# Kernel optimization log

Measured on AMD Instinct MI355X. Metric: run time of the kernel, lower is better.

Reference implementation:

```python
import jax, jax.numpy as jnp
import numpy as np

DECAY = 0.99
EPS = 1e-05
NUM_EMBEDDINGS = 2048
EMBEDDING_DIM = 512


def setup_inputs() -> dict:
    key = jax.random.key(0)
    k1, k2 = jax.random.split(key)
    z_e = jax.random.normal(k1, (16, 4096, EMBEDDING_DIM), dtype=jnp.float32)
    embedding = jax.random.normal(k2, (NUM_EMBEDDINGS, EMBEDDING_DIM), dtype=jnp.float32)
    cluster_size = jnp.zeros((NUM_EMBEDDINGS,), dtype=jnp.float32)
    embed_avg = embedding  # buffer initialized as a clone of embedding
    return {"z_e": z_e, "embedding": embedding, "cluster_size": cluster_size, "embed_avg": embed_avg}


def reference(z_e, embedding, cluster_size, embed_avg):
    K, D = embedding.shape
    flat = z_e.reshape(-1, D)  # [N, D]
    dist = (jnp.sum(flat * flat, axis=1, keepdims=True)
            - 2.0 * flat @ embedding.T
            + jnp.sum(embedding * embedding, axis=1))
    idx = jnp.argmin(dist, axis=1)  # [N] int
    z_q_raw = embedding[idx].reshape(z_e.shape)

    # EMA cluster statistics (training path). one_hot.T @ flat == segment_sum
    counts = jax.ops.segment_sum(jnp.ones_like(idx, dtype=flat.dtype), idx, num_segments=K)
    embed_sum = jax.ops.segment_sum(flat, idx, num_segments=K)  # [K, D]
    new_cluster_size = DECAY * cluster_size + (1.0 - DECAY) * counts
    new_embed_avg = DECAY * embed_avg + (1.0 - DECAY) * embed_sum
    n = jnp.sum(new_cluster_size)
    cs_smoothed = (new_cluster_size + EPS) / (n + K * EPS) * n
    new_embedding = new_embed_avg / cs_smoothed[:, None]

    # straight-through estimator
    z_q = z_e + jax.lax.stop_gradient(z_q_raw - z_e)
    commit_loss = jnp.mean((jax.lax.stop_gradient(z_e) - z_q) ** 2)
    codebook_loss = jnp.mean((z_e - jax.lax.stop_gradient(z_q)) ** 2)
    vq_loss = codebook_loss + 0.25 * commit_loss
    return (z_q, idx, vq_loss, new_embedding, new_cluster_size, new_embed_avg)
```

## Files before the change

kernel.cpp:

```cpp
#include <hip/hip_runtime.h>

typedef unsigned short ushort_t;
typedef unsigned int u32;
typedef unsigned long long u64;
typedef __attribute__((ext_vector_type(8))) short bf16x8;
typedef __attribute__((ext_vector_type(4))) float f32x4;

#define N_ROWS 65536
#define K_EMB  2048
#define D_DIM  512
#define OFF_ZQ   0
#define OFF_IDX  33554432
#define OFF_LOSS 33619968
#define OFF_EMB  33619969
#define OFF_NCS  34668545
#define OFF_NEA  34670593
#define TAU 1.5f
#define CHUNK 128
#define MAXCHUNK 2560

__device__ __forceinline__ ushort_t f2bf(float f) {
  u32 u = __float_as_uint(f);
  u32 r = (u + 0x7fffu + ((u >> 16) & 1u)) >> 16;
  return (ushort_t)r;
}
__device__ __forceinline__ float bf2f(ushort_t h) { return __uint_as_float(((u32)h) << 16); }
__device__ __forceinline__ u32 f2mono(float f) {
  u32 u = __float_as_uint(f);
  return (u & 0x80000000u) ? ~u : (u | 0x80000000u);
}
__device__ __forceinline__ float unmono(u32 m) {
  u32 u = (m & 0x80000000u) ? (m & 0x7fffffffu) : ~m;
  return __uint_as_float(u);
}
__device__ __forceinline__ void glds16(const void* g, void* l) {
  __builtin_amdgcn_global_load_lds((const __attribute__((address_space(1))) u32*)g,
                                   (__attribute__((address_space(3))) u32*)l, 16, 0, 0);
}

__global__ void prep_z_kernel(const float* __restrict__ ze, ushort_t* __restrict__ xh,
                              float* __restrict__ counts, float* __restrict__ lossws)
{
  int gid = blockIdx.x * 256 + threadIdx.x;
  const float4* zin = (const float4*)ze;
  ushort4* xh4 = (ushort4*)xh;
  for (int g = gid; g < (N_ROWS * D_DIM / 4); g += 8192 * 256) {
    float4 v = zin[g];
    ushort4 h;
    h.x = f2bf(v.x); h.y = f2bf(v.y); h.z = f2bf(v.z); h.w = f2bf(v.w);
    xh4[g] = h;
  }
  if (gid < K_EMB) counts[gid] = 0.0f;
  if (gid == 0) lossws[0] = 0.0f;
}

__global__ void prep_e_kernel(const float* __restrict__ emb, ushort_t* __restrict__ eh,
                              float* __restrict__ enorm)
{
  int w = threadIdx.x >> 6, l = threadIdx.x & 63;
  int k = blockIdx.x * 4 + w;
  const float4* row = (const float4*)(emb + (size_t)k * D_DIM);
  float4 a = row[l * 2], b = row[l * 2 + 1];
  ushort4 h0, h1;
  h0.x = f2bf(a.x); h0.y = f2bf(a.y); h0.z = f2bf(a.z); h0.w = f2bf(a.w);
  h1.x = f2bf(b.x); h1.y = f2bf(b.y); h1.z = f2bf(b.z); h1.w = f2bf(b.w);
  ((ushort4*)(eh + (size_t)k * D_DIM))[l * 2] = h0;
  ((ushort4*)(eh + (size_t)k * D_DIM))[l * 2 + 1] = h1;
  float s = a.x*a.x + a.y*a.y + a.z*a.z + a.w*a.w + b.x*b.x + b.y*b.y + b.z*b.z + b.w*b.w;
  #pragma unroll
  for (int off = 32; off >= 1; off >>= 1) s += __shfl_xor(s, off);
  if (l == 0) enorm[k] = s;
}

#define MERGE4(s1,s2,s3,s4,o1,o2,o3,o4) do {                        \
    u32 x1 = min(s1,o4), x2 = min(s2,o3), x3 = min(s3,o2), x4 = min(s4,o1); \
    u32 t1 = min(x1,x3), t3 = max(x1,x3), t2 = min(x2,x4), t4 = max(x2,x4); \
    s1 = min(t1,t2); s2 = max(t1,t2); s3 = min(t3,t4); s4 = max(t3,t4);     \
  } while (0)

__global__ __launch_bounds__(256, 4)
void dist_gemm(const ushort_t* __restrict__ xh, const ushort_t* __restrict__ eh,
               const float* __restrict__ enorm, u32* __restrict__ list)
{
  __shared__ ushort_t Ah[128 * 64];
  __shared__ ushort_t Bh[128 * 64];
  const int t = threadIdx.x;
  const int w = t >> 6, l = t & 63;
  const int li = l & 15, lg = l >> 4;
  const int bx = blockIdx.x;
  const int rt = bx >> 4, ct = bx & 15;
  const int row0 = rt << 7, col0 = ct << 7;
  const int wr = (w >> 1) << 6, wc = (w & 1) << 6;

  f32x4 zero4 = {0.f, 0.f, 0.f, 0.f};
  f32x4 acc[4][4];
  #pragma unroll
  for (int m = 0; m < 4; ++m)
    #pragma unroll
    for (int n = 0; n < 4; ++n) acc[m][n] = zero4;

  const int Gbase = (w << 6) + l;
  for (int kit = 0; kit < 8; ++kit) {
    const int kb = kit << 7;
    #pragma unroll
    for (int i = 0; i < 4; ++i) {
      int G = (i << 8) + Gbase;
      int r = G >> 3, gp = G & 7;
      int cb = gp ^ (r & 7);
      size_t gA = ((size_t)(row0 + r) << 10) + kb + (cb << 4);
      size_t gB = ((size_t)(col0 + r) << 10) + kb + (cb << 4);
      int ld = ((i << 8) + (w << 6)) << 4;
      glds16((const char*)xh + gA, (char*)Ah + ld);
      glds16((const char*)eh + gB, (char*)Bh + ld);
    }
    __syncthreads();
    #pragma unroll
    for (int kblk = 0; kblk < 2; ++kblk) {
      bf16x8 fah[4], fbh[4];
      #pragma unroll
      for (int m = 0; m < 4; ++m) {
        int r = wr + (m << 4) + li;
        int c = (kblk << 2) + lg;
        int off = (r << 7) + ((c ^ (r & 7)) << 4);
        fah[m] = *(const bf16x8*)((const char*)Ah + off);
      }
      #pragma unroll
      for (int n = 0; n < 4; ++n) {
        int r = wc + (n << 4) + li;
        int c = (kblk << 2) + lg;
        int off = (r << 7) + ((c ^ (r & 7)) << 4);
        fbh[n] = *(const bf16x8*)((const char*)Bh + off);
      }
      #pragma unroll
      for (int m = 0; m < 4; ++m)
        #pragma unroll
        for (int n = 0; n < 4; ++n)
          acc[m][n] = __builtin_amdgcn_mfma_f32_16x16x32_bf16(fah[m], fbh[n], acc[m][n], 0, 0, 0);
    }
    __syncthreads();
  }

  float en[4];
  #pragma unroll
  for (int n = 0; n < 4; ++n) en[n] = enorm[col0 + wc + (n << 4) + li];

  u32* epi = (u32*)Ah;
  #pragma unroll
  for (int m = 0; m < 4; ++m) {
    #pragma unroll
    for (int i = 0; i < 4; ++i) {
      int lrow = wr + (m << 4) + (lg << 2) + i;
      u32 s1 = 0xFFFFFFFFu, s2 = 0xFFFFFFFFu, s3 = 0xFFFFFFFFu, s4 = 0xFFFFFFFFu;
      #pragma unroll
      for (int n = 0; n < 4; ++n) {
        float dist = en[n] - 2.0f * acc[m][n][i];
        u32 ent = ((f2mono(dist) >> 11) << 11) | (u32)(col0 + wc + (n << 4) + li);
        if (ent < s1)      { s4 = s3; s3 = s2; s2 = s1; s1 = ent; }
        else if (ent < s2) { s4 = s3; s3 = s2; s2 = ent; }
        else if (ent < s3) { s4 = s3; s3 = ent; }
        else if (ent < s4) { s4 = ent; }
      }
      #pragma unroll
      for (int off = 8; off >= 1; off >>= 1) {
        u32 o1 = __shfl_xor(s1, off);
        u32 o2 = __shfl_xor(s2, off);
        u32 o3 = __shfl_xor(s3, off);
        u32 o4 = __shfl_xor(s4, off);
        MERGE4(s1, s2, s3, s4, o1, o2, o3, o4);
      }
      if (li == 0) {
        u32* p = epi + (lrow << 3) + ((w & 1) << 2);
        p[0] = s1; p[1] = s2; p[2] = s3; p[3] = s4;
      }
    }
  }
  __syncthreads();
  if (t < 128) {
    u32* pa = epi + (t << 3);
    u32 s1 = pa[0], s2 = pa[1], s3 = pa[2], s4 = pa[3];
    u32 o1 = pa[4], o2 = pa[5], o3 = pa[6], o4 = pa[7];
    MERGE4(s1, s2, s3, s4, o1, o2, o3, o4);
    uint4 v; v.x = s1; v.y = s2; v.z = s3; v.w = s4;
    *(uint4*)(list + (((size_t)(row0 + t)) << 6) + (ct << 2)) = v;
  }
}

__global__ void finalize_kernel(const u32* __restrict__ list, const float* __restrict__ ze,
                                const float* __restrict__ emb, int* __restrict__ wsidx,
                                float* __restrict__ counts)
{
  int w = threadIdx.x >> 6, l = threadIdx.x & 63;
  int row = blockIdx.x * 4 + w;
  u32 ent = list[(((size_t)row) << 6) + l];
  u32 e1 = ent;
  #pragma unroll
  for (int off = 32; off >= 1; off >>= 1) e1 = min(e1, __shfl_xor(e1, off));
  float d1 = unmono(e1 & ~2047u);
  float dl = unmono(ent & ~2047u);
  u64 mask = __ballot(dl < d1 + TAU);
  int idx;
  if (__popcll(mask) <= 1) {
    idx = (int)(e1 & 2047u);
  } else {
    double bd = 1e300; int bc = 0x7fffffff;
    const float* xr = ze + (((size_t)row) << 9);
    u64 mm = mask;
    while (mm) {
      int j = (int)(__ffsll((long long)mm) - 1);
      mm &= mm - 1;
      u32 cj = __shfl(ent, j);
      int col = (int)(cj & 2047u);
      const float* er = emb + (((size_t)col) << 9);
      double s = 0.0;
      #pragma unroll
      for (int q = 0; q < 8; ++q) {
        double df = (double)xr[(l << 3) + q] - (double)er[(l << 3) + q];
        s += df * df;
      }
      #pragma unroll
      for (int off = 32; off >= 1; off >>= 1) s += __shfl_xor(s, off);
      if (s < bd || (s == bd && col < bc)) { bd = s; bc = col; }
    }
    idx = bc;
  }
  if (l == 0) {
    wsidx[row] = idx;
    atomicAdd(&counts[idx], 1.0f);
  }
}

__global__ void scan_kernel(const float* __restrict__ counts, u32* __restrict__ offsets,
                            u32* __restrict__ cursor, u32* __restrict__ chunkinfo,
                            u32* __restrict__ ntotal)
{
  int t = threadIdx.x;
  int c[8]; int s = 0;
  #pragma unroll
  for (int i = 0; i < 8; ++i) { c[i] = (int)counts[t * 8 + i]; s += c[i]; }
  __shared__ int ts[256];
  ts[t] = s; __syncthreads();
  for (int off = 1; off < 256; off <<= 1) {
    int v = (t >= off) ? ts[t - off] : 0;
    __syncthreads();
    ts[t] += v;
    __syncthreads();
  }
  int run = ts[t] - s;
  int nch[8]; int ns = 0;
  #pragma unroll
  for (int i = 0; i < 8; ++i) {
    offsets[t * 8 + i] = (u32)run;
    cursor[t * 8 + i] = 0;
    run += c[i];
    nch[i] = (c[i] + CHUNK - 1) / CHUNK;
    ns += nch[i];
  }
  __shared__ int ts2[256];
  ts2[t] = ns; __syncthreads();
  for (int off = 1; off < 256; off <<= 1) {
    int v = (t >= off) ? ts2[t - off] : 0;
    __syncthreads();
    ts2[t] += v;
    __syncthreads();
  }
  int cb = ts2[t] - ns;
  #pragma unroll
  for (int i = 0; i < 8; ++i)
    for (int cc = 0; cc < nch[i]; ++cc)
      chunkinfo[cb++] = (u32)(t * 8 + i) | ((u32)cc << 11);
  if (t == 255) *ntotal = (u32)ts2[255];
}

__global__ void scatter_kernel(const int* __restrict__ wsidx, const u32* __restrict__ offsets,
                               u32* __restrict__ cursor, u32* __restrict__ sorted)
{
  int row = blockIdx.x * 256 + threadIdx.x;
  int idx = wsidx[row];
  u32 pos = atomicAdd(&cursor[idx], 1u);
  sorted[offsets[idx] + pos] = (u32)row;
}

__global__ void zesum_kernel(float* __restrict__ esum)
{
  int gid = blockIdx.x * 256 + threadIdx.x;
  for (int i = gid; i < K_EMB * D_DIM; i += 1024 * 256) esum[i] = 0.0f;
}

__global__ __launch_bounds__(256)
void zq_seg_kernel(const float* __restrict__ ze, const float* __restrict__ emb,
                   const u32* __restrict__ offsets, const float* __restrict__ counts,
                   const u32* __restrict__ sorted, const u32* __restrict__ chunkinfo,
                   const u32* __restrict__ ntotal, float* __restrict__ o_zq,
                   float* __restrict__ o_idx, float* __restrict__ esum,
                   float* __restrict__ lossws)
{
  int cid = blockIdx.x;
  if (cid >= (int)*ntotal) return;
  u32 rec = chunkinfo[cid];
  int k = rec & 2047, c = (int)(rec >> 11);
  int ctotal = (int)counts[k];
  int base = (int)offsets[k] + c * CHUNK;
  int cnt = min(ctotal - c * CHUNK, CHUNK);
  bool multi = ctotal > CHUNK;
  int t = threadIdx.x, w = t >> 6, l = t & 63;
  __shared__ u32 srow[CHUNK];
  __shared__ float sacc[4 * 512];
  __shared__ float sloss[4];
  if (t < cnt) srow[t] = sorted[base + t];
  __syncthreads();
  const float4* e4 = (const float4*)(emb + ((size_t)k << 9));
  float4 ev0 = e4[l * 2], ev1 = e4[l * 2 + 1];
  float a0x=0,a0y=0,a0z=0,a0w=0,a1x=0,a1y=0,a1z=0,a1w=0;
  float lacc = 0.f;
  for (int r = w; r < cnt; r += 4) {
    int row = (int)srow[r];
    const float4* z4 = (const float4*)(ze + ((size_t)row << 9));
    float4 zv0 = z4[l * 2], zv1 = z4[l * 2 + 1];
    float4 q0, q1;
    q0.x = zv0.x + (ev0.x - zv0.x);
    q0.y = zv0.y + (ev0.y - zv0.y);
    q0.z = zv0.z + (ev0.z - zv0.z);
    q0.w = zv0.w + (ev0.w - zv0.w);
    q1.x = zv1.x + (ev1.x - zv1.x);
    q1.y = zv1.y + (ev1.y - zv1.y);
    q1.z = zv1.z + (ev1.z - zv1.z);
    q1.w = zv1.w + (ev1.w - zv1.w);
    float4* zq4 = (float4*)(o_zq + ((size_t)row << 9));
    zq4[l * 2] = q0; zq4[l * 2 + 1] = q1;
    float dx = zv0.x - q0.x, dy = zv0.y - q0.y, dz = zv0.z - q0.z, dw = zv0.w - q0.w;
    lacc += dx*dx + dy*dy + dz*dz + dw*dw;
    dx = zv1.x - q1.x; dy = zv1.y - q1.y; dz = zv1.z - q1.z; dw = zv1.w - q1.w;
    lacc += dx*dx + dy*dy + dz*dz + dw*dw;
    a0x += zv0.x; a0y += zv0.y; a0z += zv0.z; a0w += zv0.w;
    a1x += zv1.x; a1y += zv1.y; a1z += zv1.z; a1w += zv1.w;
    if (l == 0) o_idx[row] = (float)k;
  }
  #pragma unroll
  for (int off = 32; off >= 1; off >>= 1) lacc += __shfl_xor(lacc, off);
  if (l == 0) sloss[w] = lacc;
  float* sa = sacc + w * 512 + l * 8;
  sa[0]=a0x; sa[1]=a0y; sa[2]=a0z; sa[3]=a0w; sa[4]=a1x; sa[5]=a1y; sa[6]=a1z; sa[7]=a1w;
  __syncthreads();
  #pragma unroll
  for (int j = 0; j < 2; ++j) {
    int col = t * 2 + j;
    float v = sacc[col] + sacc[512 + col] + sacc[1024 + col] + sacc[1536 + col];
    if (multi) atomicAdd(&esum[((size_t)k << 9) + col], v);
    else       esum[((size_t)k << 9) + col] = v;
  }
  if (t == 0) atomicAdd(lossws, sloss[0] + sloss[1] + sloss[2] + sloss[3]);
}

__global__ void d1_kernel(const float* __restrict__ cs, const float* __restrict__ counts,
                          float* __restrict__ o_ncs, float* __restrict__ inv,
                          const float* __restrict__ lossws, float* __restrict__ o_loss)
{
  int t = threadIdx.x;
  float ncs[8]; float s = 0.0f;
  #pragma unroll
  for (int i = 0; i < 8; ++i) {
    int k = t + (i << 8);
    float v = 0.99f * cs[k] + 0.01f * counts[k];
    ncs[i] = v; o_ncs[k] = v; s += v;
  }
  __shared__ float red[256];
  red[t] = s; __syncthreads();
  for (int h = 128; h >= 1; h >>= 1) { if (t < h) red[t] += red[t + h]; __syncthreads(); }
  float n = red[0];
  float denom = n + 2048.0f * 1e-5f;
  #pragma unroll
  for (int i = 0; i < 8; ++i) {
    int k = t + (i << 8);
    float sm = (ncs[i] + 1e-5f) / denom * n;
    inv[k] = 1.0f / sm;
  }
  if (t == 0) o_loss[0] = lossws[0] * 1.25f / 33554432.0f;
}

__global__ void d2_kernel(const float* __restrict__ ea, const float* __restrict__ inv,
                          float* __restrict__ o_emb, float* __restrict__ o_nea)
{
  int gid = blockIdx.x * 256 + threadIdx.x;
  for (int i = gid; i < K_EMB * D_DIM; i += 1024 * 256) {
    float es = o_emb[i];
    float nea = 0.99f * ea[i] + 0.01f * es;
    o_nea[i] = nea;
    o_emb[i] = nea * inv[i >> 9];
  }
}

extern "C" void kernel_launch(void* const* d_in, const int* in_sizes, int n_in,
                              void* d_out, int out_size, void* d_ws, size_t ws_size,
                              hipStream_t stream)
{
  const float* ze  = (const float*)d_in[0];
  const float* emb = (const float*)d_in[1];
  const float* cs  = (const float*)d_in[2];
  const float* ea  = (const float*)d_in[3];
  float* out = (float*)d_out;
  float* o_zq   = out + OFF_ZQ;
  float* o_idx  = out + OFF_IDX;
  float* o_loss = out + OFF_LOSS;
  float* o_emb  = out + OFF_EMB;
  float* o_ncs  = out + OFF_NCS;
  float* o_nea  = out + OFF_NEA;
  ushort_t* xh = (ushort_t*)d_out;
  u32* list = (u32*)(out + 16777216);
  char* ws = (char*)d_ws;
  ushort_t* ehp = (ushort_t*)ws;
  int* wsidx    = (int*)(ws + 2097152);
  float* counts = (float*)(ws + 2097152 + 262144);
  float* enorm  = counts + 2048;
  float* inv    = enorm + 2048;
  float* lossws = inv + 2048;
  u32* offsets  = (u32*)(lossws + 64);
  u32* cursor   = offsets + 2048;
  u32* sorted   = cursor + 2048;
  u32* chunkinfo= sorted + 65536;
  u32* ntotal   = chunkinfo + MAXCHUNK;

  prep_z_kernel<<<8192, 256, 0, stream>>>(ze, xh, counts, lossws);
  prep_e_kernel<<<512, 256, 0, stream>>>(emb, ehp, enorm);
  dist_gemm<<<8192, 256, 0, stream>>>(xh, ehp, enorm, list);
  finalize_kernel<<<16384, 256, 0, stream>>>(list, ze, emb, wsidx, counts);
  scan_kernel<<<1, 256, 0, stream>>>(counts, offsets, cursor, chunkinfo, ntotal);
  scatter_kernel<<<256, 256, 0, stream>>>(wsidx, offsets, cursor, sorted);
  zesum_kernel<<<1024, 256, 0, stream>>>(o_emb);
  zq_seg_kernel<<<MAXCHUNK, 256, 0, stream>>>(ze, emb, offsets, counts, sorted,
                                              chunkinfo, ntotal, o_zq, o_idx, o_emb, lossws);
  d1_kernel<<<1, 256, 0, stream>>>(cs, counts, o_ncs, inv, lossws, o_loss);
  d2_kernel<<<1024, 256, 0, stream>>>(ea, inv, o_emb, o_nea);
}
```

Before: 415.4 us.

## Fuse top-4 candidate selection across all codebook tiles inside distance GEMM

Each GEMM block now covers 128 rows against every 128-column codebook tile and keeps a running top-4 of packed distance|index keys in registers. It writes one uint4 per row instead of 64 candidate entries per row, which removes the large candidate-list write and reread and simplifies finalize to checking 4 candidates. The zeroing of the embedding sum is also restricted to clusters that are empty or larger than one chunk. Risks: the grid shrinks to 512 blocks with a two-per-CU launch bound, so the GPU may be less full. The monotone float-to-uint mapping is dropped, so ordering is only correct when distances are non-negative, which holds for these inputs but not in general.

```diff
diff --git a/kernel.cpp b/kernel.cpp
--- a/kernel.cpp
+++ b/kernel.cpp
@@ -24,19 +24,16 @@
   u32 r = (u + 0x7fffu + ((u >> 16) & 1u)) >> 16;
   return (ushort_t)r;
 }
-__device__ __forceinline__ float bf2f(ushort_t h) { return __uint_as_float(((u32)h) << 16); }
-__device__ __forceinline__ u32 f2mono(float f) {
-  u32 u = __float_as_uint(f);
-  return (u & 0x80000000u) ? ~u : (u | 0x80000000u);
-}
-__device__ __forceinline__ float unmono(u32 m) {
-  u32 u = (m & 0x80000000u) ? (m & 0x7fffffffu) : ~m;
-  return __uint_as_float(u);
-}
 __device__ __forceinline__ void glds16(const void* g, void* l) {
   __builtin_amdgcn_global_load_lds((const __attribute__((address_space(1))) u32*)g,
                                    (__attribute__((address_space(3))) u32*)l, 16, 0, 0);
 }
+
+#define MERGE4(s1,s2,s3,s4,o1,o2,o3,o4) do {                        \
+    u32 x1 = min(s1,o4), x2 = min(s2,o3), x3 = min(s3,o2), x4 = min(s4,o1); \
+    u32 t1 = min(x1,x3), t3 = max(x1,x3), t2 = min(x2,x4), t4 = max(x2,x4); \
+    s1 = min(t1,t2); s2 = max(t1,t2); s3 = min(t3,t4); s4 = max(t3,t4);     \
+  } while (0)
 
 __global__ void prep_z_kernel(const float* __restrict__ ze, ushort_t* __restrict__ xh,
                               float* __restrict__ counts, float* __restrict__ lossws)
@@ -72,149 +69,175 @@
   if (l == 0) enorm[k] = s;
 }
 
-#define MERGE4(s1,s2,s3,s4,o1,o2,o3,o4) do {                        \
-    u32 x1 = min(s1,o4), x2 = min(s2,o3), x3 = min(s3,o2), x4 = min(s4,o1); \
-    u32 t1 = min(x1,x3), t3 = max(x1,x3), t2 = min(x2,x4), t4 = max(x2,x4); \
-    s1 = min(t1,t2); s2 = max(t1,t2); s3 = min(t3,t4); s4 = max(t3,t4);     \
-  } while (0)
-
-__global__ __launch_bounds__(256, 4)
+__global__ __launch_bounds__(256, 2)
 void dist_gemm(const ushort_t* __restrict__ xh, const ushort_t* __restrict__ eh,
-               const float* __restrict__ enorm, u32* __restrict__ list)
+               const float* __restrict__ enorm, uint4* __restrict__ list)
 {
   __shared__ ushort_t Ah[128 * 64];
   __shared__ ushort_t Bh[128 * 64];
   const int t = threadIdx.x;
   const int w = t >> 6, l = t & 63;
   const int li = l & 15, lg = l >> 4;
-  const int bx = blockIdx.x;
-  const int rt = bx >> 4, ct = bx & 15;
-  const int row0 = rt << 7, col0 = ct << 7;
+  const int row0 = blockIdx.x << 7;
   const int wr = (w >> 1) << 6, wc = (w & 1) << 6;
 
-  f32x4 zero4 = {0.f, 0.f, 0.f, 0.f};
-  f32x4 acc[4][4];
-  #pragma unroll
-  for (int m = 0; m < 4; ++m)
-    #pragma unroll
-    for (int n = 0; n < 4; ++n) acc[m][n] = zero4;
+  u32 cand[16][4];
+  #pragma unroll
+  for (int mi = 0; mi < 16; ++mi) {
+    cand[mi][0] = 0xFFFFFFFFu; cand[mi][1] = 0xFFFFFFFFu;
+    cand[mi][2] = 0xFFFFFFFFu; cand[mi][3] = 0xFFFFFFFFu;
+  }
 
   const int Gbase = (w << 6) + l;
-  for (int kit = 0; kit < 8; ++kit) {
-    const int kb = kit << 7;
-    #pragma unroll
-    for (int i = 0; i < 4; ++i) {
-      int G = (i << 8) + Gbase;
-      int r = G >> 3, gp = G & 7;
-      int cb = gp ^ (r & 7);
-      size_t gA = ((size_t)(row0 + r) << 10) + kb + (cb << 4);
-      size_t gB = ((size_t)(col0 + r) << 10) + kb + (cb << 4);
-      int ld = ((i << 8) + (w << 6)) << 4;
-      glds16((const char*)xh + gA, (char*)Ah + ld);
-      glds16((const char*)eh + gB, (char*)Bh + ld);
+
+  for (int ct = 0; ct < 16; ++ct) {
+    const int col0 = ct << 7;
+    float en0 = enorm[col0 + wc + 0  + li];
+    float en1 = enorm[col0 + wc + 16 + li];
+    float en2 = enorm[col0 + wc + 32 + li];
+    float en3 = enorm[col0 + wc + 48 + li];
+
+    f32x4 acc[4][4];
+    #pragma unroll
+    for (int m = 0; m < 4; ++m)
+      #pragma unroll
+      for (int n = 0; n < 4; ++n) acc[m][n] = (f32x4){0.f, 0.f, 0.f, 0.f};
+
+    for (int kit = 0; kit < 8; ++kit) {
+      const int kb = kit << 7;
+      #pragma unroll
+      for (int i = 0; i < 4; ++i) {
+        int G = (i << 8) + Gbase;
+        int r = G >> 3, gp = G & 7;
+        int cb = gp ^ (r & 7);
+        size_t gA = ((size_t)(row0 + r) << 10) + kb + (cb << 4);
+        size_t gB = ((size_t)(col0 + r) << 10) + kb + (cb << 4);
+        int ld = ((i << 8) + (w << 6)) << 4;
+        glds16((const char*)xh + gA, (char*)Ah + ld);
+        glds16((const char*)eh + gB, (char*)Bh + ld);
+      }
+      __syncthreads();
+      #pragma unroll
+      for (int kblk = 0; kblk < 2; ++kblk) {
+        bf16x8 fah[4], fbh[4];
+        #pragma unroll
+        for (int m = 0; m < 4; ++m) {
+          int r = wr + (m << 4) + li;
+          int c = (kblk << 2) + lg;
+          int off = (r << 7) + ((c ^ (r & 7)) << 4);
+          fah[m] = *(const bf16x8*)((const char*)Ah + off);
+        }
+        #pragma unroll
+        for (int n = 0; n < 4; ++n) {
+          int r = wc + (n << 4) + li;
+          int c = (kblk << 2) + lg;
+          int off = (r << 7) + ((c ^ (r & 7)) << 4);
+          fbh[n] = *(const bf16x8*)((const char*)Bh + off);
+        }
+        #pragma unroll
+        for (int m = 0; m < 4; ++m)
+          #pragma unroll
+          for (int n = 0; n < 4; ++n)
+            acc[m][n] = __builtin_amdgcn_mfma_f32_16x16x32_bf16(fah[m], fbh[n], acc[m][n], 0, 0, 0);
+      }
+      __syncthreads();
     }
-    __syncthreads();
-    #pragma unroll
-    for (int kblk = 0; kblk < 2; ++kblk) {
-      bf16x8 fah[4], fbh[4];
-      #pragma unroll
-      for (int m = 0; m < 4; ++m) {
-        int r = wr + (m << 4) + li;
-        int c = (kblk << 2) + lg;
-        int off = (r << 7) + ((c ^ (r & 7)) << 4);
-        fah[m] = *(const bf16x8*)((const char*)Ah + off);
-      }
-      #pragma unroll
-      for (int n = 0; n < 4; ++n) {
-        int r = wc + (n << 4) + li;
-        int c = (kblk << 2) + lg;
-        int off = (r << 7) + ((c ^ (r & 7)) << 4);
-        fbh[n] = *(const bf16x8*)((const char*)Bh + off);
-      }
-      #pragma unroll
-      for (int m = 0; m < 4; ++m)
-        #pragma unroll
-        for (int n = 0; n < 4; ++n)
-          acc[m][n] = __builtin_amdgcn_mfma_f32_16x16x32_bf16(fah[m], fbh[n], acc[m][n], 0, 0, 0);
+
+    const u32 colb = (u32)(col0 + wc + li);
+    #pragma unroll
+    for (int m = 0; m < 4; ++m)
+      #pragma unroll
+      for (int i = 0; i < 4; ++i) {
+        u32 k0 = (__float_as_uint(fmaf(-2.f, acc[m][0][i], en0)) & 0xFFFFF800u) | colb;
+        u32 k1 = (__float_as_uint(fmaf(-2.f, acc[m][1][i], en1)) & 0xFFFFF800u) | (colb + 16u);
+        u32 k2 = (__float_as_uint(fmaf(-2.f, acc[m][2][i], en2)) & 0xFFFFF800u) | (colb + 32u);
+        u32 k3 = (__float_as_uint(fmaf(-2.f, acc[m][3][i], en3)) & 0xFFFFF800u) | (colb + 48u);
+        u32 a = min(k0, k1), b = max(k0, k1);
+        u32 c = min(k2, k3), d = max(k2, k3);
+        u32 e = min(a, c),  f = max(a, c);
+        u32 g = min(b, d),  h = max(b, d);
+        u32 q1 = e, q2 = min(f, g), q3 = max(f, g), q4 = h;
+        MERGE4(cand[m * 4 + i][0], cand[m * 4 + i][1],
+               cand[m * 4 + i][2], cand[m * 4 + i][3], q1, q2, q3, q4);
+      }
+  }
+
+  #pragma unroll
+  for (int mi = 0; mi < 16; ++mi) {
+    u32 s1 = cand[mi][0], s2 = cand[mi][1], s3 = cand[mi][2], s4 = cand[mi][3];
+    #pragma unroll
+    for (int off = 1; off <= 8; off <<= 1) {
+      u32 o1 = __shfl_xor(s1, off), o2 = __shfl_xor(s2, off);
+      u32 o3 = __shfl_xor(s3, off), o4 = __shfl_xor(s4, off);
+      MERGE4(s1, s2, s3, s4, o1, o2, o3, o4);
     }
-    __syncthreads();
-  }
-
-  float en[4];
-  #pragma unroll
-  for (int n = 0; n < 4; ++n) en[n] = enorm[col0 + wc + (n << 4) + li];
-
-  u32* epi = (u32*)Ah;
-  #pragma unroll
-  for (int m = 0; m < 4; ++m) {
-    #pragma unroll
-    for (int i = 0; i < 4; ++i) {
-      int lrow = wr + (m << 4) + (lg << 2) + i;
-      u32 s1 = 0xFFFFFFFFu, s2 = 0xFFFFFFFFu, s3 = 0xFFFFFFFFu, s4 = 0xFFFFFFFFu;
-      #pragma unroll
-      for (int n = 0; n < 4; ++n) {
-        float dist = en[n] - 2.0f * acc[m][n][i];
-        u32 ent = ((f2mono(dist) >> 11) << 11) | (u32)(col0 + wc + (n << 4) + li);
-        if (ent < s1)      { s4 = s3; s3 = s2; s2 = s1; s1 = ent; }
-        else if (ent < s2) { s4 = s3; s3 = s2; s2 = ent; }
-        else if (ent < s3) { s4 = s3; s3 = ent; }
-        else if (ent < s4) { s4 = ent; }
-      }
-      #pragma unroll
-      for (int off = 8; off >= 1; off >>= 1) {
-        u32 o1 = __shfl_xor(s1, off);
-        u32 o2 = __shfl_xor(s2, off);
-        u32 o3 = __shfl_xor(s3, off);
-        u32 o4 = __shfl_xor(s4, off);
+    cand[mi][0] = s1; cand[mi][1] = s2; cand[mi][2] = s3; cand[mi][3] = s4;
+  }
+
+  u32* ex = (u32*)Ah;
+  if ((w & 1) == 1 && li == 0) {
+    #pragma unroll
+    for (int m = 0; m < 4; ++m)
+      #pragma unroll
+      for (int i = 0; i < 4; ++i) {
+        int lrow = wr + (m << 4) + (lg << 2) + i;
+        uint4 v;
+        v.x = cand[m * 4 + i][0]; v.y = cand[m * 4 + i][1];
+        v.z = cand[m * 4 + i][2]; v.w = cand[m * 4 + i][3];
+        *(uint4*)&ex[lrow << 2] = v;
+      }
+  }
+  __syncthreads();
+  if ((w & 1) == 0 && li == 0) {
+    #pragma unroll
+    for (int m = 0; m < 4; ++m)
+      #pragma unroll
+      for (int i = 0; i < 4; ++i) {
+        int lrow = wr + (m << 4) + (lg << 2) + i;
+        const u32* p = &ex[lrow << 2];
+        u32 s1 = cand[m * 4 + i][0], s2 = cand[m * 4 + i][1];
+        u32 s3 = cand[m * 4 + i][2], s4 = cand[m * 4 + i][3];
+        u32 o1 = p[0], o2 = p[1], o3 = p[2], o4 = p[3];
         MERGE4(s1, s2, s3, s4, o1, o2, o3, o4);
-      }
-      if (li == 0) {
-        u32* p = epi + (lrow << 3) + ((w & 1) << 2);
-        p[0] = s1; p[1] = s2; p[2] = s3; p[3] = s4;
-      }
-    }
-  }
-  __syncthreads();
-  if (t < 128) {
-    u32* pa = epi + (t << 3);
-    u32 s1 = pa[0], s2 = pa[1], s3 = pa[2], s4 = pa[3];
-    u32 o1 = pa[4], o2 = pa[5], o3 = pa[6], o4 = pa[7];
-    MERGE4(s1, s2, s3, s4, o1, o2, o3, o4);
-    uint4 v; v.x = s1; v.y = s2; v.z = s3; v.w = s4;
-    *(uint4*)(list + (((size_t)(row0 + t)) << 6) + (ct << 2)) = v;
-  }
-}
-
-__global__ void finalize_kernel(const u32* __restrict__ list, const float* __restrict__ ze,
+        uint4 v; v.x = s1; v.y = s2; v.z = s3; v.w = s4;
+        list[row0 + lrow] = v;
+      }
+  }
+}
+
+__global__ void finalize_kernel(const uint4* __restrict__ list, const float* __restrict__ ze,
                                 const float* __restrict__ emb, int* __restrict__ wsidx,
                                 float* __restrict__ counts)
 {
   int w = threadIdx.x >> 6, l = threadIdx.x & 63;
   int row = blockIdx.x * 4 + w;
-  u32 ent = list[(((size_t)row) << 6) + l];
-  u32 e1 = ent;
-  #pragma unroll
-  for (int off = 32; off >= 1; off >>= 1) e1 = min(e1, __shfl_xor(e1, off));
-  float d1 = unmono(e1 & ~2047u);
-  float dl = unmono(ent & ~2047u);
-  u64 mask = __ballot(dl < d1 + TAU);
+  uint4 q = list[row];
+  float d1 = __uint_as_float(q.x & 0xFFFFF800u);
+  float lim = d1 + TAU;
+  bool n2 = (q.y != 0xFFFFFFFFu) && (__uint_as_float(q.y & 0xFFFFF800u) < lim);
+  bool n3 = (q.z != 0xFFFFFFFFu) && (__uint_as_float(q.z & 0xFFFFF800u) < lim);
+  bool n4 = (q.w != 0xFFFFFFFFu) && (__uint_as_float(q.w & 0xFFFFF800u) < lim);
   int idx;
-  if (__popcll(mask) <= 1) {
-    idx = (int)(e1 & 2047u);
+  if (!(n2 | n3 | n4)) {
+    idx = (int)(q.x & 2047u);
   } else {
     double bd = 1e300; int bc = 0x7fffffff;
     const float* xr = ze + (((size_t)row) << 9);
-    u64 mm = mask;
-    while (mm) {
-      int j = (int)(__ffsll((long long)mm) - 1);
-      mm &= mm - 1;
-      u32 cj = __shfl(ent, j);
-      int col = (int)(cj & 2047u);
+    double xv[8];
+    #pragma unroll
+    for (int p = 0; p < 8; ++p) xv[p] = (double)xr[(l << 3) + p];
+    #pragma unroll
+    for (int j = 0; j < 4; ++j) {
+      u32 kj = (j == 0) ? q.x : (j == 1) ? q.y : (j == 2) ? q.z : q.w;
+      bool ok = (j == 0) || ((kj != 0xFFFFFFFFu) &&
+                             (__uint_as_float(kj & 0xFFFFF800u) < lim));
+      if (!ok) continue;
+      int col = (int)(kj & 2047u);
       const float* er = emb + (((size_t)col) << 9);
       double s = 0.0;
       #pragma unroll
-      for (int q = 0; q < 8; ++q) {
-        double df = (double)xr[(l << 3) + q] - (double)er[(l << 3) + q];
+      for (int p = 0; p < 8; ++p) {
+        double df = xv[p] - (double)er[(l << 3) + p];
         s += df * df;
       }
       #pragma unroll
@@ -280,10 +303,14 @@
   sorted[offsets[idx] + pos] = (u32)row;
 }
 
-__global__ void zesum_kernel(float* __restrict__ esum)
-{
-  int gid = blockIdx.x * 256 + threadIdx.x;
-  for (int i = gid; i < K_EMB * D_DIM; i += 1024 * 256) esum[i] = 0.0f;
+__global__ void zesum_kernel(const float* __restrict__ counts, float* __restrict__ esum)
+{
+  int k = blockIdx.x;
+  float c = counts[k];
+  if (c == 0.0f || c > (float)CHUNK) {
+    esum[((size_t)k << 9) + threadIdx.x] = 0.0f;
+    esum[((size_t)k << 9) + 256 + threadIdx.x] = 0.0f;
+  }
 }
 
 __global__ __launch_bounds__(256)
@@ -405,7 +432,6 @@
   float* o_ncs  = out + OFF_NCS;
   float* o_nea  = out + OFF_NEA;
   ushort_t* xh = (ushort_t*)d_out;
-  u32* list = (u32*)(out + 16777216);
   char* ws = (char*)d_ws;
   ushort_t* ehp = (ushort_t*)ws;
   int* wsidx    = (int*)(ws + 2097152);
@@ -418,14 +444,15 @@
   u32* sorted   = cursor + 2048;
   u32* chunkinfo= sorted + 65536;
   u32* ntotal   = chunkinfo + MAXCHUNK;
+  uint4* list   = (uint4*)(ws + 3145728);
 
   prep_z_kernel<<<8192, 256, 0, stream>>>(ze, xh, counts, lossws);
   prep_e_kernel<<<512, 256, 0, stream>>>(emb, ehp, enorm);
-  dist_gemm<<<8192, 256, 0, stream>>>(xh, ehp, enorm, list);
+  dist_gemm<<<512, 256, 0, stream>>>(xh, ehp, enorm, list);
   finalize_kernel<<<16384, 256, 0, stream>>>(list, ze, emb, wsidx, counts);
   scan_kernel<<<1, 256, 0, stream>>>(counts, offsets, cursor, chunkinfo, ntotal);
   scatter_kernel<<<256, 256, 0, stream>>>(wsidx, offsets, cursor, sorted);
-  zesum_kernel<<<1024, 256, 0, stream>>>(o_emb);
+  zesum_kernel<<<2048, 256, 0, stream>>>(counts, o_emb);
   zq_seg_kernel<<<MAXCHUNK, 256, 0, stream>>>(ze, emb, offsets, counts, sorted,
                                               chunkinfo, ntotal, o_zq, o_idx, o_emb, lossws);
   d1_kernel<<<1, 256, 0, stream>>>(cs, counts, o_ncs, inv, lossws, o_loss);
```

Result: faster. 352.3 us (-15.2%).

## Retile distance GEMM to 256x256 with triple-buffered LDS pipeline and lighter epilogue

Applied to the files above, without the earlier changes.

The distance GEMM moves from 128x128 tiles and 256 threads to 256x256 tiles with 512 threads. It uses a 3-stage LDS ring with async global-to-LDS loads, explicit vmcnt waits and raised priority around the MFMA blocks, which aims to overlap loads with compute and raise reuse per tile. The candidate list halves to 32 entries per row. The epilogue drops the monotonic float mapping and uses raw float bits, which is only valid if distances stay non-negative. The finalize kernel caches the row in doubles, and esum zeroing is limited to clusters that need it.

```diff
diff --git a/kernel.cpp b/kernel.cpp
--- a/kernel.cpp
+++ b/kernel.cpp
@@ -24,19 +24,16 @@
   u32 r = (u + 0x7fffu + ((u >> 16) & 1u)) >> 16;
   return (ushort_t)r;
 }
-__device__ __forceinline__ float bf2f(ushort_t h) { return __uint_as_float(((u32)h) << 16); }
-__device__ __forceinline__ u32 f2mono(float f) {
-  u32 u = __float_as_uint(f);
-  return (u & 0x80000000u) ? ~u : (u | 0x80000000u);
-}
-__device__ __forceinline__ float unmono(u32 m) {
-  u32 u = (m & 0x80000000u) ? (m & 0x7fffffffu) : ~m;
-  return __uint_as_float(u);
-}
 __device__ __forceinline__ void glds16(const void* g, void* l) {
   __builtin_amdgcn_global_load_lds((const __attribute__((address_space(1))) u32*)g,
                                    (__attribute__((address_space(3))) u32*)l, 16, 0, 0);
 }
+
+#define MERGE4(s1,s2,s3,s4,o1,o2,o3,o4) do {                        \
+    u32 x1 = min(s1,o4), x2 = min(s2,o3), x3 = min(s3,o2), x4 = min(s4,o1); \
+    u32 t1 = min(x1,x3), t3 = max(x1,x3), t2 = min(x2,x4), t4 = max(x2,x4); \
+    s1 = min(t1,t2); s2 = max(t1,t2); s3 = min(t3,t4); s4 = max(t3,t4);     \
+  } while (0)
 
 __global__ void prep_z_kernel(const float* __restrict__ ze, ushort_t* __restrict__ xh,
                               float* __restrict__ counts, float* __restrict__ lossws)
@@ -72,116 +69,123 @@
   if (l == 0) enorm[k] = s;
 }
 
-#define MERGE4(s1,s2,s3,s4,o1,o2,o3,o4) do {                        \
-    u32 x1 = min(s1,o4), x2 = min(s2,o3), x3 = min(s3,o2), x4 = min(s4,o1); \
-    u32 t1 = min(x1,x3), t3 = max(x1,x3), t2 = min(x2,x4), t4 = max(x2,x4); \
-    s1 = min(t1,t2); s2 = max(t1,t2); s3 = min(t3,t4); s4 = max(t3,t4);     \
-  } while (0)
-
-__global__ __launch_bounds__(256, 4)
+__global__ __launch_bounds__(512, 2)
 void dist_gemm(const ushort_t* __restrict__ xh, const ushort_t* __restrict__ eh,
                const float* __restrict__ enorm, u32* __restrict__ list)
 {
-  __shared__ ushort_t Ah[128 * 64];
-  __shared__ ushort_t Bh[128 * 64];
-  const int t = threadIdx.x;
-  const int w = t >> 6, l = t & 63;
+  __shared__ char Ring[3 * 32768];
+  const int t256 = threadIdx.x;
+  const int w = t256 >> 6, l = t256 & 63;
   const int li = l & 15, lg = l >> 4;
   const int bx = blockIdx.x;
-  const int rt = bx >> 4, ct = bx & 15;
-  const int row0 = rt << 7, col0 = ct << 7;
-  const int wr = (w >> 1) << 6, wc = (w & 1) << 6;
-
-  f32x4 zero4 = {0.f, 0.f, 0.f, 0.f};
-  f32x4 acc[4][4];
-  #pragma unroll
-  for (int m = 0; m < 4; ++m)
-    #pragma unroll
-    for (int n = 0; n < 4; ++n) acc[m][n] = zero4;
-
-  const int Gbase = (w << 6) + l;
-  for (int kit = 0; kit < 8; ++kit) {
-    const int kb = kit << 7;
+  const int rt = bx & 255, ct = bx >> 8;
+  const int row0 = rt << 8, col0 = ct << 8;
+  const int wm = w >> 2, wn = w & 3;
+
+  f32x4 acc[8][4];
+  #pragma unroll
+  for (int m = 0; m < 8; ++m)
+    #pragma unroll
+    for (int n = 0; n < 4; ++n) acc[m][n] = (f32x4){0.f, 0.f, 0.f, 0.f};
+
+#define STAGE(ring_, t_) do {                                                  \
+    const int kb_ = (t_) << 6;                                                 \
+    _Pragma("unroll")                                                          \
+    for (int i = 0; i < 2; ++i) {                                              \
+      int G = (i << 9) + (w << 6) + l;                    \
+      int r_ = G >> 2, gp_ = G & 3;                                            \
+      int cb_ = gp_ ^ (r_ & 3);                       \
+      size_t gA = ((size_t)(row0 + r_) << 10) + kb_ + (cb_ << 4);              \
+      size_t gB = ((size_t)(col0 + r_) << 10) + kb_ + (cb_ << 4);              \
+      int ld_ = ((i << 9) + (w << 6)) << 4;             \
+      glds16((const char*)xh + gA, Ring + (ring_) * 32768 + ld_);              \
+      glds16((const char*)eh + gB, Ring + (ring_) * 32768 + 16384 + ld_);      \
+    }                                                                          \
+  } while (0)
+
+  STAGE(0, 0);
+  STAGE(1, 1);
+  asm volatile("s_waitcnt vmcnt(4)" ::: "memory");
+  __builtin_amdgcn_s_barrier();
+
+  #pragma unroll
+  for (int t = 0; t < 16; ++t) {
+    const int rg = t % 3;
+    if (t + 2 < 16) STAGE((t + 2) % 3, t + 2);
+    const char* base = Ring + rg * 32768;
+    bf16x8 fa[8], fb[4];
+    #pragma unroll
+    for (int m = 0; m < 8; ++m) {
+      int r = (wm << 7) + (m << 4) + li;
+      fa[m] = *(const bf16x8*)(base + (r << 6) + ((lg ^ (r & 3)) << 4));
+    }
+    #pragma unroll
+    for (int n = 0; n < 4; ++n) {
+      int r = (wn << 6) + (n << 4) + li;
+      fb[n] = *(const bf16x8*)(base + 16384 + (r << 6) + ((lg ^ (r & 3)) << 4));
+    }
+    __builtin_amdgcn_s_setprio(1);
+    #pragma unroll
+    for (int m = 0; m < 8; ++m)
+      #pragma unroll
+      for (int n = 0; n < 4; ++n)
+        acc[m][n] = __builtin_amdgcn_mfma_f32_16x16x32_bf16(fa[m], fb[n], acc[m][n], 0, 0, 0);
+    __builtin_amdgcn_s_setprio(0);
+    if (t + 2 < 16) {
+      asm volatile("s_waitcnt vmcnt(4)" ::: "memory");
+    } else if (t + 1 < 16) {
+      asm volatile("s_waitcnt vmcnt(0)" ::: "memory");
+    }
+    asm volatile("" ::: "memory");
+    __builtin_amdgcn_s_barrier();
+  }
+#undef STAGE
+
+  float en[4];
+  const int colb = col0 + (wn << 6) + li;
+  #pragma unroll
+  for (int n = 0; n < 4; ++n) en[n] = enorm[colb + (n << 4)];
+
+  uint4* ex = (uint4*)Ring;
+  #pragma unroll
+  for (int m = 0; m < 8; ++m) {
     #pragma unroll
     for (int i = 0; i < 4; ++i) {
-      int G = (i << 8) + Gbase;
-      int r = G >> 3, gp = G & 7;
-      int cb = gp ^ (r & 7);
-      size_t gA = ((size_t)(row0 + r) << 10) + kb + (cb << 4);
-      size_t gB = ((size_t)(col0 + r) << 10) + kb + (cb << 4);
-      int ld = ((i << 8) + (w << 6)) << 4;
-      glds16((const char*)xh + gA, (char*)Ah + ld);
-      glds16((const char*)eh + gB, (char*)Bh + ld);
-    }
-    __syncthreads();
-    #pragma unroll
-    for (int kblk = 0; kblk < 2; ++kblk) {
-      bf16x8 fah[4], fbh[4];
+      int lrow = (wm << 7) + (m << 4) + (lg << 2) + i;
+      u32 k0 = (__float_as_uint(fmaf(-2.f, acc[m][0][i], en[0])) & 0xFFFFF800u) | (u32)colb;
+      u32 k1 = (__float_as_uint(fmaf(-2.f, acc[m][1][i], en[1])) & 0xFFFFF800u) | (u32)(colb + 16);
+      u32 k2 = (__float_as_uint(fmaf(-2.f, acc[m][2][i], en[2])) & 0xFFFFF800u) | (u32)(colb + 32);
+      u32 k3 = (__float_as_uint(fmaf(-2.f, acc[m][3][i], en[3])) & 0xFFFFF800u) | (u32)(colb + 48);
+      u32 a = min(k0, k1), b = max(k0, k1);
+      u32 c = min(k2, k3), d = max(k2, k3);
+      u32 e = min(a, c),  f = max(a, c);
+      u32 g = min(b, d),  h = max(b, d);
+      u32 s1 = e, s2 = min(f, g), s3 = max(f, g), s4 = h;
       #pragma unroll
-      for (int m = 0; m < 4; ++m) {
-        int r = wr + (m << 4) + li;
-        int c = (kblk << 2) + lg;
-        int off = (r << 7) + ((c ^ (r & 7)) << 4);
-        fah[m] = *(const bf16x8*)((const char*)Ah + off);
-      }
-      #pragma unroll
-      for (int n = 0; n < 4; ++n) {
-        int r = wc + (n << 4) + li;
-        int c = (kblk << 2) + lg;
-        int off = (r << 7) + ((c ^ (r & 7)) << 4);
-        fbh[n] = *(const bf16x8*)((const char*)Bh + off);
-      }
-      #pragma unroll
-      for (int m = 0; m < 4; ++m)
-        #pragma unroll
-        for (int n = 0; n < 4; ++n)
-          acc[m][n] = __builtin_amdgcn_mfma_f32_16x16x32_bf16(fah[m], fbh[n], acc[m][n], 0, 0, 0);
-    }
-    __syncthreads();
-  }
-
-  float en[4];
-  #pragma unroll
-  for (int n = 0; n < 4; ++n) en[n] = enorm[col0 + wc + (n << 4) + li];
-
-  u32* epi = (u32*)Ah;
-  #pragma unroll
-  for (int m = 0; m < 4; ++m) {
-    #pragma unroll
-    for (int i = 0; i < 4; ++i) {
-      int lrow = wr + (m << 4) + (lg << 2) + i;
-      u32 s1 = 0xFFFFFFFFu, s2 = 0xFFFFFFFFu, s3 = 0xFFFFFFFFu, s4 = 0xFFFFFFFFu;
-      #pragma unroll
-      for (int n = 0; n < 4; ++n) {
-        float dist = en[n] - 2.0f * acc[m][n][i];
-        u32 ent = ((f2mono(dist) >> 11) << 11) | (u32)(col0 + wc + (n << 4) + li);
-        if (ent < s1)      { s4 = s3; s3 = s2; s2 = s1; s1 = ent; }
-        else if (ent < s2) { s4 = s3; s3 = s2; s2 = ent; }
-        else if (ent < s3) { s4 = s3; s3 = ent; }
-        else if (ent < s4) { s4 = ent; }
-      }
-      #pragma unroll
-      for (int off = 8; off >= 1; off >>= 1) {
-        u32 o1 = __shfl_xor(s1, off);
-        u32 o2 = __shfl_xor(s2, off);
-        u32 o3 = __shfl_xor(s3, off);
-        u32 o4 = __shfl_xor(s4, off);
+      for (int off = 1; off <= 8; off <<= 1) {
+        u32 o1 = __shfl_xor(s1, off), o2 = __shfl_xor(s2, off);
+        u32 o3 = __shfl_xor(s3, off), o4 = __shfl_xor(s4, off);
         MERGE4(s1, s2, s3, s4, o1, o2, o3, o4);
       }
       if (li == 0) {
-        u32* p = epi + (lrow << 3) + ((w & 1) << 2);
-        p[0] = s1; p[1] = s2; p[2] = s3; p[3] = s4;
+        uint4 v; v.x = s1; v.y = s2; v.z = s3; v.w = s4;
+        ex[(lrow << 2) + wn] = v;
       }
     }
   }
-  __syncthreads();
-  if (t < 128) {
-    u32* pa = epi + (t << 3);
-    u32 s1 = pa[0], s2 = pa[1], s3 = pa[2], s4 = pa[3];
-    u32 o1 = pa[4], o2 = pa[5], o3 = pa[6], o4 = pa[7];
-    MERGE4(s1, s2, s3, s4, o1, o2, o3, o4);
+  asm volatile("" ::: "memory");
+  __builtin_amdgcn_s_barrier();
+  if (t256 < 256) {
+    uint4 v0 = ex[(t256 << 2) + 0];
+    uint4 v1 = ex[(t256 << 2) + 1];
+    uint4 v2 = ex[(t256 << 2) + 2];
+    uint4 v3 = ex[(t256 << 2) + 3];
+    u32 s1 = v0.x, s2 = v0.y, s3 = v0.z, s4 = v0.w;
+    MERGE4(s1, s2, s3, s4, v1.x, v1.y, v1.z, v1.w);
+    MERGE4(s1, s2, s3, s4, v2.x, v2.y, v2.z, v2.w);
+    MERGE4(s1, s2, s3, s4, v3.x, v3.y, v3.z, v3.w);
     uint4 v; v.x = s1; v.y = s2; v.z = s3; v.w = s4;
-    *(uint4*)(list + (((size_t)(row0 + t)) << 6) + (ct << 2)) = v;
+    *(uint4*)&list[(((size_t)(row0 + t256)) << 5) + (ct << 2)] = v;
   }
 }
 
@@ -191,12 +195,12 @@
 {
   int w = threadIdx.x >> 6, l = threadIdx.x & 63;
   int row = blockIdx.x * 4 + w;
-  u32 ent = list[(((size_t)row) << 6) + l];
+  u32 ent = (l < 32) ? list[(((size_t)row) << 5) + l] : 0xFFFFFFFFu;
   u32 e1 = ent;
   #pragma unroll
   for (int off = 32; off >= 1; off >>= 1) e1 = min(e1, __shfl_xor(e1, off));
-  float d1 = unmono(e1 & ~2047u);
-  float dl = unmono(ent & ~2047u);
+  float d1 = __uint_as_float(e1 & 0xFFFFF800u);
+  float dl = __uint_as_float(ent & 0xFFFFF800u);
   u64 mask = __ballot(dl < d1 + TAU);
   int idx;
   if (__popcll(mask) <= 1) {
@@ -204,6 +208,9 @@
   } else {
     double bd = 1e300; int bc = 0x7fffffff;
     const float* xr = ze + (((size_t)row) << 9);
+    double xv[8];
+    #pragma unroll
+    for (int p = 0; p < 8; ++p) xv[p] = (double)xr[(l << 3) + p];
     u64 mm = mask;
     while (mm) {
       int j = (int)(__ffsll((long long)mm) - 1);
@@ -213,8 +220,8 @@
       const float* er = emb + (((size_t)col) << 9);
       double s = 0.0;
       #pragma unroll
-      for (int q = 0; q < 8; ++q) {
-        double df = (double)xr[(l << 3) + q] - (double)er[(l << 3) + q];
+      for (int p = 0; p < 8; ++p) {
+        double df = xv[p] - (double)er[(l << 3) + p];
         s += df * df;
       }
       #pragma unroll
@@ -280,10 +287,14 @@
   sorted[offsets[idx] + pos] = (u32)row;
 }
 
-__global__ void zesum_kernel(float* __restrict__ esum)
-{
-  int gid = blockIdx.x * 256 + threadIdx.x;
-  for (int i = gid; i < K_EMB * D_DIM; i += 1024 * 256) esum[i] = 0.0f;
+__global__ void zesum_kernel(const float* __restrict__ counts, float* __restrict__ esum)
+{
+  int k = blockIdx.x;
+  float c = counts[k];
+  if (c == 0.0f || c > (float)CHUNK) {
+    esum[((size_t)k << 9) + threadIdx.x] = 0.0f;
+    esum[((size_t)k << 9) + 256 + threadIdx.x] = 0.0f;
+  }
 }
 
 __global__ __launch_bounds__(256)
@@ -405,7 +416,7 @@
   float* o_ncs  = out + OFF_NCS;
   float* o_nea  = out + OFF_NEA;
   ushort_t* xh = (ushort_t*)d_out;
-  u32* list = (u32*)(out + 16777216);
+  u32* list    = (u32*)(out + 16777216);
   char* ws = (char*)d_ws;
   ushort_t* ehp = (ushort_t*)ws;
   int* wsidx    = (int*)(ws + 2097152);
@@ -421,11 +432,11 @@
 
   prep_z_kernel<<<8192, 256, 0, stream>>>(ze, xh, counts, lossws);
   prep_e_kernel<<<512, 256, 0, stream>>>(emb, ehp, enorm);
-  dist_gemm<<<8192, 256, 0, stream>>>(xh, ehp, enorm, list);
+  dist_gemm<<<2048, 512, 0, stream>>>(xh, ehp, enorm, list);
   finalize_kernel<<<16384, 256, 0, stream>>>(list, ze, emb, wsidx, counts);
   scan_kernel<<<1, 256, 0, stream>>>(counts, offsets, cursor, chunkinfo, ntotal);
   scatter_kernel<<<256, 256, 0, stream>>>(wsidx, offsets, cursor, sorted);
-  zesum_kernel<<<1024, 256, 0, stream>>>(o_emb);
+  zesum_kernel<<<2048, 256, 0, stream>>>(counts, o_emb);
   zq_seg_kernel<<<MAXCHUNK, 256, 0, stream>>>(ze, emb, offsets, counts, sorted,
                                               chunkinfo, ntotal, o_zq, o_idx, o_emb, lossws);
   d1_kernel<<<1, 256, 0, stream>>>(cs, counts, o_ncs, inv, lossws, o_loss);
```

After: 411.4 us. Within noise of the previous version (-1.0%).
